# Performance work log

Measured on AMD Instinct MI355X. Metric: run time of the kernel, lower is better.

The kernel has to match this reference:

```python
import jax, jax.numpy as jnp
import numpy as np

N_NODES = 100000


def _gcn_layer(x, src, dst, ew, norm_s, norm_d, W, b):
    # DGL GraphConv with edge weights, norm='both':
    # h_v = D_in(v)^-1/2 * sum_{(u,v) in E} w_uv * D_out(u)^-1/2 * x_u; then Linear.
    m = (x * norm_s[:, None])[src] * ew[:, None]        # [E, d] gather + weight
    agg = jax.ops.segment_sum(m, dst, num_segments=N_NODES)  # [N, d] scatter-add
    return (agg * norm_d[:, None]) @ W + b


def setup_inputs() -> dict:
    key = jax.random.key(0)
    ks = jax.random.split(key, 12)
    N, E, D, C = N_NODES, 1600000, 64, 32
    inp = {
        "x": jax.random.normal(ks[0], (N, D), jnp.float32),
        "src": jax.random.randint(ks[1], (E,), 0, N, jnp.int64),
        "dst": jax.random.randint(ks[2], (E,), 0, N, jnp.int64),
        "ew": jax.random.uniform(ks[3], (E,), jnp.float32),
    }
    s = 1.0 / np.sqrt(D)
    for i, k in zip(range(1, 5), ks[4:8]):
        inp[f"W{i}"] = jax.random.normal(k, (D, D), jnp.float32) * s
        inp[f"b{i}"] = jnp.zeros((D,), jnp.float32)
    inp["Wr"] = jax.random.normal(ks[8], (D, D), jnp.float32) * s
    inp["br"] = jnp.zeros((D,), jnp.float32)
    inp["Wo"] = jax.random.normal(ks[9], (D, C), jnp.float32) * s
    inp["bo"] = jnp.zeros((C,), jnp.float32)
    return inp


def reference(x, src, dst, ew, W1, b1, W2, b2, W3, b3, W4, b4, Wr, br, Wo, bo):
    ones = jnp.ones(src.shape, x.dtype)
    deg_out = jnp.clip(jax.ops.segment_sum(ones, src, num_segments=N_NODES), 1.0)
    deg_in = jnp.clip(jax.ops.segment_sum(ones, dst, num_segments=N_NODES), 1.0)
    norm_s = deg_out ** -0.5
    norm_d = deg_in ** -0.5

    res = x @ Wr + br
    h = jax.nn.relu(_gcn_layer(x, src, dst, ew, norm_s, norm_d, W1, b1))
    h = jax.nn.relu(_gcn_layer(h, src, dst, ew, norm_s, norm_d, W2, b2))
    h = jax.nn.relu(_gcn_layer(h, src, dst, ew, norm_s, norm_d, W3, b3))
    h = _gcn_layer(h, src, dst, ew, norm_s, norm_d, W4, b4)
    h = jax.nn.relu(h + res)
    return h @ Wo + bo
```

## Files before the change

### kernel.cpp

```cpp
#include <hip/hip_runtime.h>

#define NN 100000
#define D 64
#define G 3
#define RS 33334
#define NC 85
#define NB (G*NC)

typedef short bf16x8 __attribute__((ext_vector_type(8)));
typedef float f32x4 __attribute__((ext_vector_type(4)));
typedef float f32x2 __attribute__((ext_vector_type(2)));

__device__ __forceinline__ float bf2f_lo(unsigned w) { return __uint_as_float(w << 16); }
__device__ __forceinline__ float bf2f_hi(unsigned w) { return __uint_as_float(w & 0xffff0000u); }
__device__ __forceinline__ unsigned short f2bf(float f) {
    unsigned u = __float_as_uint(f);
    return (unsigned short)((u + 0x7fffu + ((u >> 16) & 1u)) >> 16);
}
__device__ __forceinline__ unsigned pack2(float a, float b) {
    return (unsigned)f2bf(a) | ((unsigned)f2bf(b) << 16);
}
__device__ __forceinline__ unsigned char f2fp8(float v) {
    return (unsigned char)(__builtin_amdgcn_cvt_pk_fp8_f32(v, v, 0, false) & 0xff);
}
__device__ __forceinline__ unsigned pack_cw(int s, float w) {
    return ((unsigned)f2bf(w) << 17) | (unsigned)s;
}
#define PKFMA(acc, w2, p) \
    asm("v_pk_fma_f32 %0, %1, %2, %0" : "+v"(acc) : "v"(w2), "v"(p))

__global__ __launch_bounds__(1024) void k_hist(const int* __restrict__ src,
                                               const int* __restrict__ dst,
                                               unsigned short* __restrict__ psd, int E) {
    __shared__ unsigned h[RS / 2];
    int b = blockIdx.x, t = threadIdx.x;
    int g = b / NC, c = b - g * NC;
    int lo = g * RS;
    for (int i = t; i < RS / 2; i += 1024) h[i] = 0;
    __syncthreads();
    int e0 = (int)((((long long)c * E / NC)) & ~3LL);
    int e1 = (c == NC - 1) ? E : (int)((((long long)(c + 1) * E / NC)) & ~3LL);
    int m = (e1 - e0) & ~4095;
    for (int e = e0 + t * 4; e < e0 + m; e += 4096) {
        int4 s4 = *(const int4*)(src + e);
        int4 d4 = *(const int4*)(dst + e);
        int v;
        v = s4.x - lo; if ((unsigned)v < RS) atomicAdd(&h[v >> 1], 1u << ((v & 1) * 16));
        v = s4.y - lo; if ((unsigned)v < RS) atomicAdd(&h[v >> 1], 1u << ((v & 1) * 16));
        v = s4.z - lo; if ((unsigned)v < RS) atomicAdd(&h[v >> 1], 1u << ((v & 1) * 16));
        v = s4.w - lo; if ((unsigned)v < RS) atomicAdd(&h[v >> 1], 1u << ((v & 1) * 16));
        v = d4.x - lo; if ((unsigned)v < RS) atomicAdd(&h[v >> 1], 1u << ((v & 1) * 16 + 8));
        v = d4.y - lo; if ((unsigned)v < RS) atomicAdd(&h[v >> 1], 1u << ((v & 1) * 16 + 8));
        v = d4.z - lo; if ((unsigned)v < RS) atomicAdd(&h[v >> 1], 1u << ((v & 1) * 16 + 8));
        v = d4.w - lo; if ((unsigned)v < RS) atomicAdd(&h[v >> 1], 1u << ((v & 1) * 16 + 8));
    }
    for (int e = e0 + m + t; e < e1; e += 1024) {
        int v = src[e] - lo; if ((unsigned)v < RS) atomicAdd(&h[v >> 1], 1u << ((v & 1) * 16));
        v = dst[e] - lo;     if ((unsigned)v < RS) atomicAdd(&h[v >> 1], 1u << ((v & 1) * 16 + 8));
    }
    __syncthreads();
    unsigned* pb = (unsigned*)(psd + (size_t)b * RS);
    for (int i = t; i < RS / 2; i += 1024) pb[i] = h[i];
}

__global__ __launch_bounds__(1024) void k_scan1m(const unsigned short* __restrict__ psd,
                                                 float* __restrict__ ns, float* __restrict__ nd,
                                                 int* __restrict__ rowptr,
                                                 int* __restrict__ bsum, int n) {
    __shared__ int lds[1024];
    int t = threadIdx.x;
    int i = blockIdx.x * 1024 + t;
    int sv = 0, dv = 0;
    if (i < n) {
        int g = i / RS, off = i - g * RS;
        const unsigned short* p = psd + (size_t)(g * NC) * RS + off;
        #pragma unroll 5
        for (int c = 0; c < NC; ++c) {
            unsigned v = p[(size_t)c * RS];
            sv += (int)(v & 0xffu);
            dv += (int)(v >> 8);
        }
        ns[i] = rsqrtf(fmaxf((float)sv, 1.0f));
        nd[i] = rsqrtf(fmaxf((float)dv, 1.0f));
    }
    lds[t] = dv;
    __syncthreads();
    for (int off = 1; off < 1024; off <<= 1) {
        int v = lds[t];
        int a = (t >= off) ? lds[t - off] : 0;
        __syncthreads();
        lds[t] = v + a;
        __syncthreads();
    }
    if (t == 1023) bsum[blockIdx.x] = lds[1023];
    if (i < n) rowptr[i] = lds[t] - dv;
}

__global__ void k_scan3c(int* __restrict__ rowptr, const int* __restrict__ bsum,
                         const unsigned short* __restrict__ psd,
                         unsigned short* __restrict__ cur16,
                         int n, int E, int nb) {
    __shared__ int sbs[128];
    int t = threadIdx.x;
    if (t < 128) sbs[t] = (t < nb) ? bsum[t] : 0;
    __syncthreads();
    for (int off = 1; off < 128; off <<= 1) {
        int v = 0, a = 0;
        if (t < 128) { v = sbs[t]; if (t >= off) a = sbs[t - off]; }
        __syncthreads();
        if (t < 128) sbs[t] = v + a;
        __syncthreads();
    }
    int i = blockIdx.x * blockDim.x + t;
    if (i == 0) rowptr[n] = E;
    if (i >= n) return;
    int blk = i >> 10;
    int base = (blk > 0) ? sbs[blk - 1] : 0;
    int r = rowptr[i] + base;
    rowptr[i] = r;
    int g = i / RS, off = i - g * RS;
    const unsigned short* p = psd + (size_t)(g * NC) * RS + off;
    unsigned short* cp = cur16 + (size_t)(g * NC) * RS + off;
    int run = 0;
    #pragma unroll 5
    for (int c = 0; c < NC; ++c) {
        cp[(size_t)c * RS] = (unsigned short)run;
        run += (int)(p[(size_t)c * RS] >> 8);
    }
}

__global__ __launch_bounds__(1024) void k_fillsort(const int* __restrict__ src,
                                                   const int* __restrict__ dst,
                                                   const float* __restrict__ ew,
                                                   const int* __restrict__ rowptr,
                                                   const unsigned short* __restrict__ cur16,
                                                   unsigned* __restrict__ cw, int E) {
    __shared__ int cur[RS];
    int b = blockIdx.x, t = threadIdx.x;
    int g = b / NC, c = b - g * NC;
    int lo = g * RS;
    const unsigned short* c16 = cur16 + (size_t)b * RS;
    for (int i = t; i < RS; i += 1024) cur[i] = rowptr[lo + i] + (int)c16[i];
    __syncthreads();
    int e0 = (int)((((long long)c * E / NC)) & ~3LL);
    int e1 = (c == NC - 1) ? E : (int)((((long long)(c + 1) * E / NC)) & ~3LL);
    int m = (e1 - e0) & ~4095;
    for (int e = e0 + t * 4; e < e0 + m; e += 4096) {
        int4 s4 = *(const int4*)(src + e);
        int4 d4 = *(const int4*)(dst + e);
        float4 w4 = *(const float4*)(ew + e);
        int d;
        d = d4.x - lo; if ((unsigned)d < RS) { int p = atomicAdd(&cur[d], 1); cw[p] = pack_cw(s4.x, w4.x); }
        d = d4.y - lo; if ((unsigned)d < RS) { int p = atomicAdd(&cur[d], 1); cw[p] = pack_cw(s4.y, w4.y); }
        d = d4.z - lo; if ((unsigned)d < RS) { int p = atomicAdd(&cur[d], 1); cw[p] = pack_cw(s4.z, w4.z); }
        d = d4.w - lo; if ((unsigned)d < RS) { int p = atomicAdd(&cur[d], 1); cw[p] = pack_cw(s4.w, w4.w); }
    }
    for (int e = e0 + m + t; e < e1; e += 1024) {
        int d = dst[e] - lo;
        if ((unsigned)d < RS) {
            int p = atomicAdd(&cur[d], 1);
            cw[p] = pack_cw(src[e], ew[e]);
        }
    }
}

__global__ __launch_bounds__(256) void k_gemm2(const float* __restrict__ x,
                                               const float* __restrict__ Wr,
                                               const float* __restrict__ brs,
                                               const float* __restrict__ W1,
                                               const float* __restrict__ ns,
                                               unsigned short* __restrict__ resb,
                                               unsigned char* __restrict__ tmat, int n) {
    __shared__ unsigned short WTr[64][72];
    __shared__ unsigned short WT1[64][72];
    int t = threadIdx.x;
    for (int i = t; i < 64 * 64; i += 256) {
        int k = i >> 6, nn = i & 63;
        WTr[nn][k] = f2bf(Wr[i]);
        WT1[nn][k] = f2bf(W1[i]);
    }
    __syncthreads();
    int w = t >> 6, lane = t & 63;
    int m = lane & 15, q = lane >> 4;
    int node0 = blockIdx.x * 64 + w * 16;
    int nodeA = min(node0 + m, n - 1);
    const float* inf = x + (size_t)nodeA * D;
    float sc = ns[nodeA];
    bf16x8 afr[2], afs[2];
    #pragma unroll
    for (int kc = 0; kc < 2; ++kc) {
        float4 f0 = *(const float4*)(inf + kc * 32 + q * 8);
        float4 f1 = *(const float4*)(inf + kc * 32 + q * 8 + 4);
        union { bf16x8 v; unsigned short u[8]; } ta, ts;
        ta.u[0] = f2bf(f0.x); ta.u[1] = f2bf(f0.y);
        ta.u[2] = f2bf(f0.z); ta.u[3] = f2bf(f0.w);
        ta.u[4] = f2bf(f1.x); ta.u[5] = f2bf(f1.y);
        ta.u[6] = f2bf(f1.z); ta.u[7] = f2bf(f1.w);
        ts.u[0] = f2bf(f0.x * sc); ts.u[1] = f2bf(f0.y * sc);
        ts.u[2] = f2bf(f0.z * sc); ts.u[3] = f2bf(f0.w * sc);
        ts.u[4] = f2bf(f1.x * sc); ts.u[5] = f2bf(f1.y * sc);
        ts.u[6] = f2bf(f1.z * sc); ts.u[7] = f2bf(f1.w * sc);
        afr[kc] = ta.v;
        afs[kc] = ts.v;
    }
    #pragma unroll
    for (int nt = 0; nt < 4; ++nt) {
        f32x4 ar = {0.f, 0.f, 0.f, 0.f};
        f32x4 at = {0.f, 0.f, 0.f, 0.f};
        #pragma unroll
        for (int kc = 0; kc < 2; ++kc) {
            union { bf16x8 v; uint4 u; } bfr, bf1;
            bfr.u = *(const uint4*)&WTr[nt * 16 + m][kc * 32 + q * 8];
            bf1.u = *(const uint4*)&WT1[nt * 16 + m][kc * 32 + q * 8];
            ar = __builtin_amdgcn_mfma_f32_16x16x32_bf16(afr[kc], bfr.v, ar, 0, 0, 0);
            at = __builtin_amdgcn_mfma_f32_16x16x32_bf16(afs[kc], bf1.v, at, 0, 0, 0);
        }
        int col = nt * 16 + m;
        float bb = brs[col];
        #pragma unroll
        for (int r = 0; r < 4; ++r) {
            int node = node0 + q * 4 + r;
            if (node < n) {
                resb[(size_t)node * D + col] = f2bf(ar[r] + bb);
                tmat[(size_t)node * D + col] = f2fp8(at[r]);
            }
        }
    }
}

template<bool LAST>
__global__ void k_gather(const int* __restrict__ rowptr, const unsigned* __restrict__ cw,
                         const unsigned char* __restrict__ tmat,
                         const float* __restrict__ nd, const float* __restrict__ ns,
                         const float* __restrict__ bias,
                         const unsigned short* __restrict__ resb,
                         unsigned short* __restrict__ outb, int n, int E) {
    int node = blockIdx.x * (blockDim.x >> 5) + (threadIdx.x >> 5);
    int lane = threadIdx.x & 31;
    if (node >= n) return;
    int g = lane >> 3;
    int h = lane & 7;
    int beg = rowptr[node], end = rowptr[node + 1];
    f32x2 A0 = {0.f, 0.f}, A1 = {0.f, 0.f}, A2 = {0.f, 0.f}, A3 = {0.f, 0.f};
    f32x2 C0 = {0.f, 0.f}, C1 = {0.f, 0.f}, C2 = {0.f, 0.f}, C3 = {0.f, 0.f};
    int e0 = beg + g;
    unsigned cvA = (e0      < end) ? cw[e0]      : 0u;
    unsigned cvB = (e0 + 4  < end) ? cw[e0 + 4]  : 0u;
    unsigned cvC = (e0 + 8  < end) ? cw[e0 + 8]  : 0u;
    unsigned cvD = (e0 + 12 < end) ? cw[e0 + 12] : 0u;
    for (int base = beg; base < end; base += 16) {
        uint2 rA = *((const uint2*)(tmat + (size_t)(cvA & 0x1FFFFu) * D) + h);
        uint2 rB = *((const uint2*)(tmat + (size_t)(cvB & 0x1FFFFu) * D) + h);
        uint2 rC = *((const uint2*)(tmat + (size_t)(cvC & 0x1FFFFu) * D) + h);
        uint2 rD = *((const uint2*)(tmat + (size_t)(cvD & 0x1FFFFu) * D) + h);
        int f0 = base + 16 + g;
        unsigned nvA = (f0      < end) ? cw[f0]      : 0u;
        unsigned nvB = (f0 + 4  < end) ? cw[f0 + 4]  : 0u;
        unsigned nvC = (f0 + 8  < end) ? cw[f0 + 8]  : 0u;
        unsigned nvD = (f0 + 12 < end) ? cw[f0 + 12] : 0u;
        float wA = __uint_as_float((cvA >> 17) << 16);
        float wB = __uint_as_float((cvB >> 17) << 16);
        float wC = __uint_as_float((cvC >> 17) << 16);
        float wD = __uint_as_float((cvD >> 17) << 16);
        f32x2 w2A = {wA, wA}, w2B = {wB, wB}, w2C = {wC, wC}, w2D = {wD, wD};
        f32x2 p;
        p = __builtin_amdgcn_cvt_pk_f32_fp8(rA.x, false); PKFMA(A0, w2A, p);
        p = __builtin_amdgcn_cvt_pk_f32_fp8(rA.x, true);  PKFMA(A1, w2A, p);
        p = __builtin_amdgcn_cvt_pk_f32_fp8(rA.y, false); PKFMA(A2, w2A, p);
        p = __builtin_amdgcn_cvt_pk_f32_fp8(rA.y, true);  PKFMA(A3, w2A, p);
        p = __builtin_amdgcn_cvt_pk_f32_fp8(rB.x, false); PKFMA(C0, w2B, p);
        p = __builtin_amdgcn_cvt_pk_f32_fp8(rB.x, true);  PKFMA(C1, w2B, p);
        p = __builtin_amdgcn_cvt_pk_f32_fp8(rB.y, false); PKFMA(C2, w2B, p);
        p = __builtin_amdgcn_cvt_pk_f32_fp8(rB.y, true);  PKFMA(C3, w2B, p);
        p = __builtin_amdgcn_cvt_pk_f32_fp8(rC.x, false); PKFMA(A0, w2C, p);
        p = __builtin_amdgcn_cvt_pk_f32_fp8(rC.x, true);  PKFMA(A1, w2C, p);
        p = __builtin_amdgcn_cvt_pk_f32_fp8(rC.y, false); PKFMA(A2, w2C, p);
        p = __builtin_amdgcn_cvt_pk_f32_fp8(rC.y, true);  PKFMA(A3, w2C, p);
        p = __builtin_amdgcn_cvt_pk_f32_fp8(rD.x, false); PKFMA(C0, w2D, p);
        p = __builtin_amdgcn_cvt_pk_f32_fp8(rD.x, true);  PKFMA(C1, w2D, p);
        p = __builtin_amdgcn_cvt_pk_f32_fp8(rD.y, false); PKFMA(C2, w2D, p);
        p = __builtin_amdgcn_cvt_pk_f32_fp8(rD.y, true);  PKFMA(C3, w2D, p);
        cvA = nvA; cvB = nvB; cvC = nvC; cvD = nvD;
    }
    float a0 = A0.x + C0.x, a1 = A0.y + C0.y;
    float a2 = A1.x + C1.x, a3 = A1.y + C1.y;
    float a4 = A2.x + C2.x, a5 = A2.y + C2.y;
    float a6 = A3.x + C3.x, a7 = A3.y + C3.y;
    #pragma unroll
    for (int msk = 8; msk <= 16; msk <<= 1) {
        a0 += __shfl_xor(a0, msk); a1 += __shfl_xor(a1, msk);
        a2 += __shfl_xor(a2, msk); a3 += __shfl_xor(a3, msk);
        a4 += __shfl_xor(a4, msk); a5 += __shfl_xor(a5, msk);
        a6 += __shfl_xor(a6, msk); a7 += __shfl_xor(a7, msk);
    }
    float ndv = nd[node];
    float4 b0 = *(const float4*)(bias + 8 * h);
    float4 b1 = *(const float4*)(bias + 8 * h + 4);
    float v0 = ndv * a0 + b0.x, v1 = ndv * a1 + b0.y;
    float v2 = ndv * a2 + b0.z, v3 = ndv * a3 + b0.w;
    float v4 = ndv * a4 + b1.x, v5 = ndv * a5 + b1.y;
    float v6 = ndv * a6 + b1.z, v7 = ndv * a7 + b1.w;
    if (LAST) {
        uint4 r = *((const uint4*)(resb + (size_t)node * D) + h);
        v0 += bf2f_lo(r.x); v1 += bf2f_hi(r.x);
        v2 += bf2f_lo(r.y); v3 += bf2f_hi(r.y);
        v4 += bf2f_lo(r.z); v5 += bf2f_hi(r.z);
        v6 += bf2f_lo(r.w); v7 += bf2f_hi(r.w);
    }
    v0 = fmaxf(v0, 0.f); v1 = fmaxf(v1, 0.f); v2 = fmaxf(v2, 0.f); v3 = fmaxf(v3, 0.f);
    v4 = fmaxf(v4, 0.f); v5 = fmaxf(v5, 0.f); v6 = fmaxf(v6, 0.f); v7 = fmaxf(v7, 0.f);
    if (!LAST) {
        float s = ns[node];
        v0 *= s; v1 *= s; v2 *= s; v3 *= s; v4 *= s; v5 *= s; v6 *= s; v7 *= s;
    }
    if (g == 0) {
        uint4 o = make_uint4(pack2(v0, v1), pack2(v2, v3), pack2(v4, v5), pack2(v6, v7));
        *((uint4*)(outb + (size_t)node * D) + h) = o;
    }
}

template<int OUTD, bool BIAS, int OUTMODE>
__global__ __launch_bounds__(256) void k_gemm(const unsigned short* __restrict__ inb,
                                              const float* __restrict__ W,
                                              const float* __restrict__ bias,
                                              void* __restrict__ out_, int n) {
    constexpr int NT = OUTD / 16;
    __shared__ unsigned short WT[OUTD][72];
    int t = threadIdx.x;
    for (int i = t; i < 64 * OUTD; i += 256) {
        int k = i / OUTD, nn = i % OUTD;
        WT[nn][k] = f2bf(W[i]);
    }
    __syncthreads();
    int w = t >> 6, lane = t & 63;
    int m = lane & 15, q = lane >> 4;
    int node0 = blockIdx.x * 64 + w * 16;
    int nodeA = min(node0 + m, n - 1);
    const unsigned short* ip = inb + (size_t)nodeA * D;
    bf16x8 afr[2];
    #pragma unroll
    for (int kc = 0; kc < 2; ++kc) {
        union { bf16x8 v; uint4 u; } tmp;
        tmp.u = *(const uint4*)(ip + kc * 32 + q * 8);
        afr[kc] = tmp.v;
    }
    #pragma unroll
    for (int nt = 0; nt < NT; ++nt) {
        f32x4 acc = {0.f, 0.f, 0.f, 0.f};
        #pragma unroll
        for (int kc = 0; kc < 2; ++kc) {
            union { bf16x8 v; uint4 u; } bfr;
            bfr.u = *(const uint4*)&WT[nt * 16 + m][kc * 32 + q * 8];
            acc = __builtin_amdgcn_mfma_f32_16x16x32_bf16(afr[kc], bfr.v, acc, 0, 0, 0);
        }
        int col = nt * 16 + m;
        float bb = BIAS ? bias[col] : 0.f;
        #pragma unroll
        for (int r = 0; r < 4; ++r) {
            int node = node0 + q * 4 + r;
            if (node < n) {
                float v = acc[r] + bb;
                if (OUTMODE == 2)
                    ((unsigned char*)out_)[(size_t)node * OUTD + col] = f2fp8(v);
                else
                    ((float*)out_)[(size_t)node * OUTD + col] = v;
            }
        }
    }
}

static inline char* align_up(char* p, size_t a) {
    return (char*)(((uintptr_t)p + a - 1) & ~(uintptr_t)(a - 1));
}

extern "C" void kernel_launch(void* const* d_in, const int* in_sizes, int n_in,
                              void* d_out, int out_size, void* d_ws, size_t ws_size,
                              hipStream_t stream) {
    const float* x   = (const float*)d_in[0];
    const int*   src = (const int*)d_in[1];
    const int*   dst = (const int*)d_in[2];
    const float* ew  = (const float*)d_in[3];
    const float* Wl[4] = {(const float*)d_in[4], (const float*)d_in[6],
                          (const float*)d_in[8], (const float*)d_in[10]};
    const float* bl[4] = {(const float*)d_in[5], (const float*)d_in[7],
                          (const float*)d_in[9], (const float*)d_in[11]};
    const float* Wr = (const float*)d_in[12];
    const float* br = (const float*)d_in[13];
    const float* Wo = (const float*)d_in[14];
    const float* bo = (const float*)d_in[15];
    float* out = (float*)d_out;

    const int N = NN;
    const int E = in_sizes[1];

    char* p = (char*)d_ws;
    float* norm_s = (float*)p;            p = align_up(p + N * 4, 256);
    float* norm_d = (float*)p;            p = align_up(p + N * 4, 256);
    int*   rowptr = (int*)p;              p = align_up(p + (size_t)(G * RS + 80) * 4, 256);
    int*   bsum   = (int*)p;              p = align_up(p + 128 * 4, 256);
    unsigned* cw  = (unsigned*)p;         p = align_up(p + (size_t)E * 4, 256);
    unsigned short* psd   = (unsigned short*)p; p = align_up(p + (size_t)NB * RS * 2, 256);
    unsigned short* cur16 = (unsigned short*)p; p = align_up(p + (size_t)NB * RS * 2, 256);
    unsigned short* resb  = (unsigned short*)p; p = align_up(p + (size_t)N * D * 2, 256);
    unsigned short* xs   = psd;
    unsigned char*  tmat = (unsigned char*)(xs + (size_t)N * D);

    k_hist<<<NB, 1024, 0, stream>>>(src, dst, psd, E);
    int nb = (N + 1023) / 1024;
    k_scan1m<<<nb, 1024, 0, stream>>>(psd, norm_s, norm_d, rowptr, bsum, N);
    k_scan3c<<<(N + 255) / 256, 256, 0, stream>>>(rowptr, bsum, psd, cur16, N, E, nb);
    k_fillsort<<<NB, 1024, 0, stream>>>(src, dst, ew, rowptr, cur16, cw, E);

    k_gemm2<<<(N + 63) / 64, 256, 0, stream>>>(x, Wr, br, Wl[0], norm_s, resb, tmat, N);

    k_gather<false><<<(N + 7) / 8, 256, 0, stream>>>(
        rowptr, cw, tmat, norm_d, norm_s, bl[0], nullptr, xs, N, E);
    k_gemm<64, false, 2><<<(N + 63) / 64, 256, 0, stream>>>(xs, Wl[1], nullptr, tmat, N);
    k_gather<false><<<(N + 7) / 8, 256, 0, stream>>>(
        rowptr, cw, tmat, norm_d, norm_s, bl[1], nullptr, xs, N, E);
    k_gemm<64, false, 2><<<(N + 63) / 64, 256, 0, stream>>>(xs, Wl[2], nullptr, tmat, N);
    k_gather<false><<<(N + 7) / 8, 256, 0, stream>>>(
        rowptr, cw, tmat, norm_d, norm_s, bl[2], nullptr, xs, N, E);
    k_gemm<64, false, 2><<<(N + 63) / 64, 256, 0, stream>>>(xs, Wl[3], nullptr, tmat, N);
    k_gather<true><<<(N + 7) / 8, 256, 0, stream>>>(
        rowptr, cw, tmat, norm_d, nullptr, bl[3], resb, xs, N, E);
    k_gemm<32, true, 0><<<(N + 63) / 64, 256, 0, stream>>>(xs, Wo, bo, out, N);
}
```

Baseline: 323.7 us.

## Assign one node per 8-lane group in gather, dropping cross-group shuffle reduction

The gather kernel now maps each node to 8 lanes instead of 32, with each lane group walking all of the node's edges four at a time rather than splitting edges across four sub-groups. This removes the xor-shuffle reduction and the single-group store, and puts four times as many nodes in each block. In exchange there is less memory-level parallelism per node and more load imbalance between lanes of a wave when degrees differ. Out-of-range nodes now stay in the loop with an empty edge range until the final return.

```diff
diff --git a/kernel.cpp b/kernel.cpp
--- a/kernel.cpp
+++ b/kernel.cpp
@@ -235,29 +235,30 @@
                          const float* __restrict__ bias,
                          const unsigned short* __restrict__ resb,
                          unsigned short* __restrict__ outb, int n, int E) {
-    int node = blockIdx.x * (blockDim.x >> 5) + (threadIdx.x >> 5);
-    int lane = threadIdx.x & 31;
-    if (node >= n) return;
-    int g = lane >> 3;
-    int h = lane & 7;
-    int beg = rowptr[node], end = rowptr[node + 1];
-    f32x2 A0 = {0.f, 0.f}, A1 = {0.f, 0.f}, A2 = {0.f, 0.f}, A3 = {0.f, 0.f};
-    f32x2 C0 = {0.f, 0.f}, C1 = {0.f, 0.f}, C2 = {0.f, 0.f}, C3 = {0.f, 0.f};
-    int e0 = beg + g;
-    unsigned cvA = (e0      < end) ? cw[e0]      : 0u;
-    unsigned cvB = (e0 + 4  < end) ? cw[e0 + 4]  : 0u;
-    unsigned cvC = (e0 + 8  < end) ? cw[e0 + 8]  : 0u;
-    unsigned cvD = (e0 + 12 < end) ? cw[e0 + 12] : 0u;
-    for (int base = beg; base < end; base += 16) {
-        uint2 rA = *((const uint2*)(tmat + (size_t)(cvA & 0x1FFFFu) * D) + h);
-        uint2 rB = *((const uint2*)(tmat + (size_t)(cvB & 0x1FFFFu) * D) + h);
-        uint2 rC = *((const uint2*)(tmat + (size_t)(cvC & 0x1FFFFu) * D) + h);
-        uint2 rD = *((const uint2*)(tmat + (size_t)(cvD & 0x1FFFFu) * D) + h);
-        int f0 = base + 16 + g;
-        unsigned nvA = (f0      < end) ? cw[f0]      : 0u;
-        unsigned nvB = (f0 + 4  < end) ? cw[f0 + 4]  : 0u;
-        unsigned nvC = (f0 + 8  < end) ? cw[f0 + 8]  : 0u;
-        unsigned nvD = (f0 + 12 < end) ? cw[f0 + 12] : 0u;
+    int grp = threadIdx.x >> 3;
+    int h   = threadIdx.x & 7;
+    int node = blockIdx.x * 32 + grp;
+    bool valid = node < n;
+    int nc = valid ? node : 0;
+    int beg = rowptr[nc];
+    int end = valid ? rowptr[nc + 1] : beg;
+    unsigned h8 = (unsigned)(h * 8);
+    f32x2 A0={0.f,0.f},A1={0.f,0.f},A2={0.f,0.f},A3={0.f,0.f};
+    f32x2 C0={0.f,0.f},C1={0.f,0.f},C2={0.f,0.f},C3={0.f,0.f};
+    unsigned cvA = (beg     < end) ? cw[beg]     : 0u;
+    unsigned cvB = (beg + 1 < end) ? cw[beg + 1] : 0u;
+    unsigned cvC = (beg + 2 < end) ? cw[beg + 2] : 0u;
+    unsigned cvD = (beg + 3 < end) ? cw[beg + 3] : 0u;
+    for (int e = beg; e < end; e += 4) {
+        uint2 rA = *(const uint2*)(tmat + (((cvA & 0x1FFFFu) << 6) + h8));
+        uint2 rB = *(const uint2*)(tmat + (((cvB & 0x1FFFFu) << 6) + h8));
+        uint2 rC = *(const uint2*)(tmat + (((cvC & 0x1FFFFu) << 6) + h8));
+        uint2 rD = *(const uint2*)(tmat + (((cvD & 0x1FFFFu) << 6) + h8));
+        int f = e + 4;
+        unsigned nvA = (f     < end) ? cw[f]     : 0u;
+        unsigned nvB = (f + 1 < end) ? cw[f + 1] : 0u;
+        unsigned nvC = (f + 2 < end) ? cw[f + 2] : 0u;
+        unsigned nvD = (f + 3 < end) ? cw[f + 3] : 0u;
         float wA = __uint_as_float((cvA >> 17) << 16);
         float wB = __uint_as_float((cvB >> 17) << 16);
         float wC = __uint_as_float((cvC >> 17) << 16);
@@ -282,17 +283,11 @@
         p = __builtin_amdgcn_cvt_pk_f32_fp8(rD.y, true);  PKFMA(C3, w2D, p);
         cvA = nvA; cvB = nvB; cvC = nvC; cvD = nvD;
     }
+    if (!valid) return;
     float a0 = A0.x + C0.x, a1 = A0.y + C0.y;
     float a2 = A1.x + C1.x, a3 = A1.y + C1.y;
     float a4 = A2.x + C2.x, a5 = A2.y + C2.y;
     float a6 = A3.x + C3.x, a7 = A3.y + C3.y;
-    #pragma unroll
-    for (int msk = 8; msk <= 16; msk <<= 1) {
-        a0 += __shfl_xor(a0, msk); a1 += __shfl_xor(a1, msk);
-        a2 += __shfl_xor(a2, msk); a3 += __shfl_xor(a3, msk);
-        a4 += __shfl_xor(a4, msk); a5 += __shfl_xor(a5, msk);
-        a6 += __shfl_xor(a6, msk); a7 += __shfl_xor(a7, msk);
-    }
     float ndv = nd[node];
     float4 b0 = *(const float4*)(bias + 8 * h);
     float4 b1 = *(const float4*)(bias + 8 * h + 4);
@@ -313,10 +308,8 @@
         float s = ns[node];
         v0 *= s; v1 *= s; v2 *= s; v3 *= s; v4 *= s; v5 *= s; v6 *= s; v7 *= s;
     }
-    if (g == 0) {
-        uint4 o = make_uint4(pack2(v0, v1), pack2(v2, v3), pack2(v4, v5), pack2(v6, v7));
-        *((uint4*)(outb + (size_t)node * D) + h) = o;
-    }
+    uint4 o = make_uint4(pack2(v0, v1), pack2(v2, v3), pack2(v4, v5), pack2(v6, v7));
+    *((uint4*)(outb + (size_t)node * D) + h) = o;
 }
 
 template<int OUTD, bool BIAS, int OUTMODE>
@@ -413,16 +406,16 @@
 
     k_gemm2<<<(N + 63) / 64, 256, 0, stream>>>(x, Wr, br, Wl[0], norm_s, resb, tmat, N);
 
-    k_gather<false><<<(N + 7) / 8, 256, 0, stream>>>(
+    k_gather<false><<<(N + 31) / 32, 256, 0, stream>>>(
         rowptr, cw, tmat, norm_d, norm_s, bl[0], nullptr, xs, N, E);
     k_gemm<64, false, 2><<<(N + 63) / 64, 256, 0, stream>>>(xs, Wl[1], nullptr, tmat, N);
-    k_gather<false><<<(N + 7) / 8, 256, 0, stream>>>(
+    k_gather<false><<<(N + 31) / 32, 256, 0, stream>>>(
         rowptr, cw, tmat, norm_d, norm_s, bl[1], nullptr, xs, N, E);
     k_gemm<64, false, 2><<<(N + 63) / 64, 256, 0, stream>>>(xs, Wl[2], nullptr, tmat, N);
-    k_gather<false><<<(N + 7) / 8, 256, 0, stream>>>(
+    k_gather<false><<<(N + 31) / 32, 256, 0, stream>>>(
         rowptr, cw, tmat, norm_d, norm_s, bl[2], nullptr, xs, N, E);
     k_gemm<64, false, 2><<<(N + 63) / 64, 256, 0, stream>>>(xs, Wl[3], nullptr, tmat, N);
-    k_gather<true><<<(N + 7) / 8, 256, 0, stream>>>(
+    k_gather<true><<<(N + 31) / 32, 256, 0, stream>>>(
         rowptr, cw, tmat, norm_d, nullptr, bl[3], resb, xs, N, E);
     k_gemm<32, true, 0><<<(N + 63) / 64, 256, 0, stream>>>(xs, Wo, bo, out, N);
 }
```

Measured after the change: 310.3 us. -4.1%, faster.
